# Optimization experiments

Hardware: AMD Instinct MI355X
Metric: run time of the kernel (lower is better)

## Reference

```python
import jax, jax.numpy as jnp
import numpy as np

MD = 4                  # corr_md
D = 2 * MD + 1          # patch_size = 9


def setup_inputs() -> dict:
    key = jax.random.key(0)
    k1, k2 = jax.random.split(key)
    b, c, h, w = 4, 128, 128, 256
    t1 = jax.random.normal(k1, (b, c, h, w), dtype=jnp.float32)
    t2 = jax.random.normal(k2, (b, c, h, w), dtype=jnp.float32)
    return {"t1": t1, "t2": t2}


def reference(t1, t2):
    # Local cost volume: for each displacement (di, dj) in [-MD, MD]^2,
    # out[b, p, y, x] = sum_c t1[b, c, y, x] * t2[b, c, y+di, x+dj]
    # with zero padding outside t2 (SpatialCorrelationSampler semantics,
    # kernel_size=1, stride=1, dilation_patch=1; no channel normalization).
    b, c, h, w = t1.shape
    t2p = jnp.pad(t2, ((0, 0), (0, 0), (MD, MD), (MD, MD)))
    # Loop over the fixed 9x9 displacement grid (81 small reductions);
    outs = [
        jnp.einsum('bchw,bchw->bhw', t1, t2p[:, :, i:i + h, j:j + w])
        for i in range(D) for j in range(D)
    ]
    return jnp.stack(outs, axis=1)  # [b, 81, h, w]
```

## Files before the change

### kernel.cpp

```cpp
#include <hip/hip_runtime.h>

#define NP 81
#define CC 128
#define HH 128
#define WW 256
#define SX 24
#define NXT 11
#define NBLK (NXT * 16 * 4)

typedef __attribute__((ext_vector_type(8))) short short8;
typedef __attribute__((ext_vector_type(4))) float f32x4;
typedef __attribute__((ext_vector_type(16))) float f32x16;

__device__ __forceinline__ short f2bf(float f) {
    unsigned int u = __builtin_bit_cast(unsigned int, f);
    u += 0x7fffu + ((u >> 16) & 1u);
    return (short)(u >> 16);
}

__global__ __launch_bounds__(1024) void corr_fused24(
        const float* __restrict__ t1, const float* __restrict__ t2,
        float* __restrict__ out) {
    const int bid = blockIdx.x;
    const int sw  = (bid & 7) * (NBLK / 8) + (bid >> 3);
    const int ys = sw & 15;
    const int v  = sw >> 4;
    const int xt = v % NXT;
    const int b  = v / NXT;
    const int X0 = xt * SX;
    const int y0 = ys * 8;

    const int tid  = threadIdx.x;
    const int lane = tid & 63;
    const int w    = tid >> 6;
    const int n    = lane & 31;
    const int g    = lane >> 5;

    __shared__ short sA[8 * SX * 128];
    __shared__ __align__(16) float obufs[16 * 9 * 28];

    const size_t plane = (size_t)HH * WW;
    const int r = y0 - 4 + w;

    short8 bre[8];
    {
        const int x2 = X0 - 4 + n;
        if (r >= 0 && r < HH && x2 >= 0 && x2 < WW) {
            const float* p = t2 + ((size_t)(b * CC + g * 8) * HH + r) * WW + x2;
#pragma unroll
            for (int kc = 0; kc < 8; ++kc) {
                short8 f;
#pragma unroll
                for (int j = 0; j < 8; ++j)
                    f[j] = f2bf(p[(size_t)(kc * 16 + j) * plane]);
                bre[kc] = f;
            }
        } else {
#pragma unroll
            for (int kc = 0; kc < 8; ++kc)
                bre[kc] = (short8){0,0,0,0,0,0,0,0};
        }
    }

#pragma unroll
    for (int i = 0; i < 3; ++i) {
        const int unit = tid + i * 1024;
        const int x    = unit % SX;
        const int rest = unit / SX;
        const int oct  = rest & 15;
        const int yy   = rest >> 4;
        short8 pk = {0,0,0,0,0,0,0,0};
        if (X0 + x < WW) {
            const float* p = t1 + ((size_t)(b * CC + oct * 8) * HH + (y0 + yy)) * WW
                           + X0 + x;
#pragma unroll
            for (int j = 0; j < 8; ++j) pk[j] = f2bf(p[(size_t)j * plane]);
        }
        *(short8*)&sA[yy * (SX * 128) + x * 128 + ((oct ^ (x & 15)) * 8)] = pk;
    }
    __syncthreads();

    const int ylo = (w > 8) ? (w - 8) : 0;
    const int yhi = (w < 7) ? w : 7;
    float* ob = &obufs[w * 252];

    for (int yy = ylo; yy <= yhi; ++yy) {
        const int sbase = yy * (SX * 128) + n * 128;

        f32x16 a;
#pragma unroll
        for (int q = 0; q < 16; ++q) a[q] = 0.f;
#pragma unroll
        for (int kc = 0; kc < 8; ++kc) {
            const short8 af = *(const short8*)
                &sA[sbase + (((kc * 2 + g) ^ (n & 15)) * 8)];
            a = __builtin_amdgcn_mfma_f32_32x32x16_bf16(af, bre[kc], a, 0, 0, 0);
        }

#pragma unroll
        for (int q = 0; q < 16; ++q) {
            const int m  = (q & 3) + 8 * (q >> 2) + 4 * g;
            const int dj = n - m;
            if (dj >= 0 && dj <= 8 && m < SX) ob[dj * 28 + m] = a[q];
        }

        const int di = w - yy;
        const int y  = y0 + yy;
        if (lane < 54) {
            const int dj = lane / 6, xq = lane % 6;
            if (X0 + xq * 4 < WW) {
                f32x4 vv = *(const f32x4*)&ob[dj * 28 + xq * 4];
                *(f32x4*)&out[((size_t)(b * NP + di * 9 + dj) * HH + y) * WW
                              + X0 + xq * 4] = vv;
            }
        }
    }
}

extern "C" void kernel_launch(void* const* d_in, const int* in_sizes, int n_in,
                              void* d_out, int out_size, void* d_ws, size_t ws_size,
                              hipStream_t stream) {
    const float* t1 = (const float*)d_in[0];
    const float* t2 = (const float*)d_in[1];
    corr_fused24<<<NBLK, 1024, 0, stream>>>(t1, t2, (float*)d_out);
}
```

Measured before the change: 190.5 us.

## Prepass t2 into padded channel-last bf16 workspace; vectorize t1 staging loads

Adds a prepass kernel that converts t2 to bf16 and transposes it into a zero-padded channel-innermost workspace, so the main kernel can load its B fragments as contiguous 16-byte reads with no bounds checks. The t1 staging in the main kernel now uses float4 loads along x instead of strided scalar loads across channels. This removes the uncoalesced, plane-strided gathers of t2, which were repeated for every tile. The cost is an extra launch and a write and reread of the roughly 38 MB bf16 workspace. The original kernel is kept as a fallback when the workspace is too small.

```diff
diff --git a/kernel.cpp b/kernel.cpp
--- a/kernel.cpp
+++ b/kernel.cpp
@@ -7,6 +7,9 @@
 #define SX 24
 #define NXT 11
 #define NBLK (NXT * 16 * 4)
+#define YPAD 136
+#define XPAD 272
+#define WS_NEED (4ull * YPAD * XPAD * CC * 2ull)
 
 typedef __attribute__((ext_vector_type(8))) short short8;
 typedef __attribute__((ext_vector_type(4))) float f32x4;
@@ -18,7 +21,138 @@
     return (short)(u >> 16);
 }
 
-__global__ __launch_bounds__(1024) void corr_fused24(
+__global__ __launch_bounds__(256) void prepass_t2t(const float* __restrict__ t2,
+                                                   short* __restrict__ ws) {
+    const int blk = blockIdx.x;
+    const int yp  = blk % YPAD;
+    const int b   = blk / YPAD;
+    const int tid = threadIdx.x;
+    short* wrow = ws + (size_t)blk * XPAD * CC;
+    const int y2 = yp - 4;
+    const short8 z = {0, 0, 0, 0, 0, 0, 0, 0};
+    if (y2 < 0 || y2 >= HH) {
+        for (int u = tid; u < XPAD * CC / 8; u += 256)
+            *(short8*)&wrow[(size_t)u * 8] = z;
+        return;
+    }
+    __shared__ short sT[64 * 136];
+    {
+        const int xh = tid >> 4;
+        const int xp = (xh < 4) ? xh : xh + 256;
+        *(short8*)&wrow[(size_t)xp * CC + (tid & 15) * 8] = z;
+    }
+    const int c   = tid & 127;
+    const int x4h = tid >> 7;
+    const int oct = tid & 15;
+    const int xr  = tid >> 4;
+    const float* prow = t2 + ((size_t)(b * CC + c) * HH + y2) * WW;
+    for (int ch = 0; ch < 4; ++ch) {
+        const int xbase = ch * 64;
+#pragma unroll
+        for (int rr = 0; rr < 8; ++rr) {
+            const int x4 = x4h + 2 * rr;
+            const f32x4 vv = *(const f32x4*)&prow[xbase + x4 * 4];
+#pragma unroll
+            for (int j = 0; j < 4; ++j)
+                sT[(x4 * 4 + j) * 136 + c] = f2bf(vv[j]);
+        }
+        __syncthreads();
+#pragma unroll
+        for (int r2 = 0; r2 < 4; ++r2) {
+            const int x = xr + 16 * r2;
+            const short8 vv = *(const short8*)&sT[x * 136 + oct * 8];
+            *(short8*)&wrow[(size_t)(xbase + x + 4) * CC + oct * 8] = vv;
+        }
+        __syncthreads();
+    }
+}
+
+__global__ __launch_bounds__(1024) void corr_main24(
+        const float* __restrict__ t1, const short* __restrict__ ws,
+        float* __restrict__ out) {
+    const int bid = blockIdx.x;
+    const int sw  = (bid & 7) * (NBLK / 8) + (bid >> 3);
+    const int ys = sw & 15;
+    const int v  = sw >> 4;
+    const int xt = v % NXT;
+    const int b  = v / NXT;
+    const int X0 = xt * SX;
+    const int y0 = ys * 8;
+
+    const int tid  = threadIdx.x;
+    const int lane = tid & 63;
+    const int w    = tid >> 6;
+    const int n    = lane & 31;
+    const int g    = lane >> 5;
+
+    __shared__ short sA[8 * SX * 128];
+    __shared__ __align__(16) float obufs[16 * 9 * 28];
+
+    const short* bp = ws + ((size_t)(b * YPAD + y0 + w) * XPAD + X0 + n) * CC
+                    + g * 8;
+    short8 bre[8];
+#pragma unroll
+    for (int kc = 0; kc < 8; ++kc)
+        bre[kc] = *(const short8*)&bp[kc * 16];
+
+#pragma unroll
+    for (int i = 0; i < 6; ++i) {
+        const int idx = tid + i * 1024;
+        const int x4 = idx % 6;
+        const int vv = idx / 6;
+        const int c  = vv & 127;
+        const int yy = vv >> 7;
+        const int xg = X0 + x4 * 4;
+        f32x4 t = {0.f, 0.f, 0.f, 0.f};
+        if (xg < WW)
+            t = *(const f32x4*)&t1[((size_t)(b * CC + c) * HH + y0 + yy) * WW + xg];
+        const int oct = c >> 3;
+#pragma unroll
+        for (int j = 0; j < 4; ++j) {
+            const int x = x4 * 4 + j;
+            sA[yy * 3072 + x * 128 + ((oct ^ (x & 15)) * 8 + (c & 7))] = f2bf(t[j]);
+        }
+    }
+    __syncthreads();
+
+    const int ylo = (w > 8) ? (w - 8) : 0;
+    const int yhi = (w < 7) ? w : 7;
+    float* ob = &obufs[w * 252];
+
+    for (int yy = ylo; yy <= yhi; ++yy) {
+        const int sbase = yy * 3072 + n * 128;
+
+        f32x16 a;
+#pragma unroll
+        for (int q = 0; q < 16; ++q) a[q] = 0.f;
+#pragma unroll
+        for (int kc = 0; kc < 8; ++kc) {
+            const short8 af = *(const short8*)
+                &sA[sbase + (((kc * 2 + g) ^ (n & 15)) * 8)];
+            a = __builtin_amdgcn_mfma_f32_32x32x16_bf16(af, bre[kc], a, 0, 0, 0);
+        }
+
+#pragma unroll
+        for (int q = 0; q < 16; ++q) {
+            const int m  = (q & 3) + 8 * (q >> 2) + 4 * g;
+            const int dj = n - m;
+            if (dj >= 0 && dj <= 8 && m < SX) ob[dj * 28 + m] = a[q];
+        }
+
+        const int di = w - yy;
+        const int y  = y0 + yy;
+        if (lane < 54) {
+            const int dj = lane / 6, xq = lane % 6;
+            if (X0 + xq * 4 < WW) {
+                f32x4 vv = *(const f32x4*)&ob[dj * 28 + xq * 4];
+                *(f32x4*)&out[((size_t)(b * NP + di * 9 + dj) * HH + y) * WW
+                              + X0 + xq * 4] = vv;
+            }
+        }
+    }
+}
+
+__global__ __launch_bounds__(1024) void corr_fallback(
         const float* __restrict__ t1, const float* __restrict__ t2,
         float* __restrict__ out) {
     const int bid = blockIdx.x;
@@ -29,39 +163,15 @@
     const int b  = v / NXT;
     const int X0 = xt * SX;
     const int y0 = ys * 8;
-
     const int tid  = threadIdx.x;
     const int lane = tid & 63;
     const int w    = tid >> 6;
     const int n    = lane & 31;
     const int g    = lane >> 5;
-
     __shared__ short sA[8 * SX * 128];
     __shared__ __align__(16) float obufs[16 * 9 * 28];
-
     const size_t plane = (size_t)HH * WW;
     const int r = y0 - 4 + w;
-
-    short8 bre[8];
-    {
-        const int x2 = X0 - 4 + n;
-        if (r >= 0 && r < HH && x2 >= 0 && x2 < WW) {
-            const float* p = t2 + ((size_t)(b * CC + g * 8) * HH + r) * WW + x2;
-#pragma unroll
-            for (int kc = 0; kc < 8; ++kc) {
-                short8 f;
-#pragma unroll
-                for (int j = 0; j < 8; ++j)
-                    f[j] = f2bf(p[(size_t)(kc * 16 + j) * plane]);
-                bre[kc] = f;
-            }
-        } else {
-#pragma unroll
-            for (int kc = 0; kc < 8; ++kc)
-                bre[kc] = (short8){0,0,0,0,0,0,0,0};
-        }
-    }
-
 #pragma unroll
     for (int i = 0; i < 3; ++i) {
         const int unit = tid + i * 1024;
@@ -79,14 +189,25 @@
         *(short8*)&sA[yy * (SX * 128) + x * 128 + ((oct ^ (x & 15)) * 8)] = pk;
     }
     __syncthreads();
-
+    const int x2 = X0 - 4 + n;
+    const bool ok = (r >= 0) && (r < HH) && (x2 >= 0) && (x2 < WW);
+    const int rc  = r  < 0 ? 0 : (r  > HH - 1 ? HH - 1 : r);
+    const int xc  = x2 < 0 ? 0 : (x2 > WW - 1 ? WW - 1 : x2);
+    const float* bp = t2 + ((size_t)(b * CC + g * 8) * HH + rc) * WW + xc;
+    short8 bre[8];
+#pragma unroll
+    for (int kc = 0; kc < 8; ++kc) {
+        short8 f;
+#pragma unroll
+        for (int j = 0; j < 8; ++j) f[j] = f2bf(bp[(size_t)(kc * 16 + j) * plane]);
+        if (!ok) f = (short8){0,0,0,0,0,0,0,0};
+        bre[kc] = f;
+    }
     const int ylo = (w > 8) ? (w - 8) : 0;
     const int yhi = (w < 7) ? w : 7;
     float* ob = &obufs[w * 252];
-
     for (int yy = ylo; yy <= yhi; ++yy) {
         const int sbase = yy * (SX * 128) + n * 128;
-
         f32x16 a;
 #pragma unroll
         for (int q = 0; q < 16; ++q) a[q] = 0.f;
@@ -96,14 +217,12 @@
                 &sA[sbase + (((kc * 2 + g) ^ (n & 15)) * 8)];
             a = __builtin_amdgcn_mfma_f32_32x32x16_bf16(af, bre[kc], a, 0, 0, 0);
         }
-
 #pragma unroll
         for (int q = 0; q < 16; ++q) {
             const int m  = (q & 3) + 8 * (q >> 2) + 4 * g;
             const int dj = n - m;
             if (dj >= 0 && dj <= 8 && m < SX) ob[dj * 28 + m] = a[q];
         }
-
         const int di = w - yy;
         const int y  = y0 + yy;
         if (lane < 54) {
@@ -122,5 +241,11 @@
                               hipStream_t stream) {
     const float* t1 = (const float*)d_in[0];
     const float* t2 = (const float*)d_in[1];
-    corr_fused24<<<NBLK, 1024, 0, stream>>>(t1, t2, (float*)d_out);
-}
+    if (ws_size >= WS_NEED) {
+        short* ws = (short*)d_ws;
+        prepass_t2t<<<4 * YPAD, 256, 0, stream>>>(t2, ws);
+        corr_main24<<<NBLK, 1024, 0, stream>>>(t1, ws, (float*)d_out);
+    } else {
+        corr_fallback<<<NBLK, 1024, 0, stream>>>(t1, t2, (float*)d_out);
+    }
+}
```

After: 210.2 us. 1.1x slower.
